# Kernel optimization log

Hardware: AMD Instinct MI355X
Metric: run time of the kernel (lower is better)

Reference implementation:

```python
import jax, jax.numpy as jnp
import numpy as np

HIDDEN, NOISE, MLPW, NCOND, DATA, INIT_NOISE = 64, 16, 128, 4, 8, 16
T, B = 128, 8192
TSCALE = 1.0


def _lipswish(x):
    return 0.909 * x * jax.nn.sigmoid(x)


def _mlp(x, Ws, bs):
    for W, b in zip(Ws[:-1], bs[:-1]):
        x = _lipswish(x @ W + b)
    return TSCALE * jnp.tanh(x @ Ws[-1] + bs[-1])  # tanh regularization, tscale=1.0


def setup_inputs():
    key = jax.random.key(0)
    ks = jax.random.split(key, 12)

    def lin(k, fi, fo):
        k1, k2 = jax.random.split(k)
        lim = 1.0 / float(np.sqrt(fi))
        W = jax.random.uniform(k1, (fi, fo), minval=-lim, maxval=lim, dtype=jnp.float32)
        b = jax.random.uniform(k2, (fo,), minval=-lim, maxval=lim, dtype=jnp.float32)
        return W, b

    ind = 1 + HIDDEN + NCOND  # cat([t, x, c0])
    dr_W0, dr_b0 = lin(ks[0], ind, MLPW)
    dr_W1, dr_b1 = lin(ks[1], MLPW, MLPW)
    dr_W2, dr_b2 = lin(ks[2], MLPW, HIDDEN)
    di_W0, di_b0 = lin(ks[3], ind, MLPW)
    di_W1, di_b1 = lin(ks[4], MLPW, MLPW)
    di_W2, di_b2 = lin(ks[5], MLPW, HIDDEN * NOISE)
    init_W, init_b = lin(ks[6], INIT_NOISE + NCOND, HIDDEN)
    ro_W, ro_b = lin(ks[7], HIDDEN + NCOND, DATA)

    ts = jnp.linspace(0.0, 1.0, T, dtype=jnp.float32)
    dt = 1.0 / (T - 1)
    dW = jax.random.normal(ks[8], (T - 1, B, NOISE), dtype=jnp.float32) * float(np.sqrt(dt))
    conditions = jax.random.normal(ks[9], (NCOND,), dtype=jnp.float32)
    return dict(ts=ts, conditions=conditions, dW=dW,
                dr_W0=dr_W0, dr_b0=dr_b0, dr_W1=dr_W1, dr_b1=dr_b1, dr_W2=dr_W2, dr_b2=dr_b2,
                di_W0=di_W0, di_b0=di_b0, di_W1=di_W1, di_b1=di_b1, di_W2=di_W2, di_b2=di_b2,
                init_W=init_W, init_b=init_b, ro_W=ro_W, ro_b=ro_b, batch_size=B)


def reference(ts, conditions, dW, dr_W0, dr_b0, dr_W1, dr_b1, dr_W2, dr_b2,
              di_W0, di_b0, di_W1, di_b1, di_W2, di_b2, init_W, init_b, ro_W, ro_b,
              batch_size):
    drWs, drbs = (dr_W0, dr_W1, dr_W2), (dr_b0, dr_b1, dr_b2)
    diWs, dibs = (di_W0, di_W1, di_W2), (di_b0, di_b1, di_b2)

    h0 = jnp.ones((batch_size, INIT_NOISE), jnp.float32)  # fixed=True initial point
    c0 = jnp.broadcast_to(conditions[None, :], (batch_size, NCOND))
    x0 = jnp.concatenate([h0, c0], 1) @ init_W + init_b  # (B, H)

    def fg(t, x):
        tcol = jnp.full((x.shape[0], 1), t, x.dtype)
        tx = jnp.concatenate([tcol, x, c0], 1)
        f = _mlp(tx, drWs, drbs)  # (B, H)
        g = _mlp(tx, diWs, dibs).reshape(x.shape[0], HIDDEN, NOISE)  # (B, H, M)
        return f, g

    f0, g0 = fg(ts[0], x0)
    dts = jnp.diff(ts)

    def step(carry, inp):
        y, z, fz, gz = carry
        t1, dt, dw = inp
        # reversible Heun (Stratonovich): auxiliary state z, re-used (f,g) at (t_n, z_n)
        z1 = 2.0 * y - z + fz * dt + jnp.einsum('bhm,bm->bh', gz, dw)
        f1, g1 = fg(t1, z1)
        y1 = y + 0.5 * dt * (fz + f1) + 0.5 * jnp.einsum('bhm,bm->bh', gz + g1, dw)
        return (y1, z1, f1, g1), y1

    _, ys = jax.lax.scan(step, (x0, x0, f0, g0), (ts[1:], dts, dW))
    xs = jnp.concatenate([x0[None], ys], 0).transpose(1, 0, 2)  # (B, T, H)
    nT = xs.shape[1]
    cs = jnp.broadcast_to(c0[:, None, :], (batch_size, nT, NCOND))
    out = jnp.concatenate([xs, cs], -1) @ ro_W + ro_b  # (B, T, data)
    ts_e = jnp.broadcast_to(ts[None, :, None], (batch_size, nT, 1))
    # linear_interpolation_coeffs with no NaNs is the identity on the values
    return jnp.concatenate([ts_e, out], -1)  # (B, T, 1 + data)
```

## Files before the change

kernel.cpp:

```cpp
#include <hip/hip_runtime.h>
#include <hip/hip_bf16.h>
#include <cstdint>
#include <cstddef>

#define B_TOT   8192
#define T_TOT   128
#define ROWS    32
#define THREADS 1024
#define DT      (1.0f/127.0f)

typedef __bf16 bf16x8 __attribute__((ext_vector_type(8)));
typedef float  f32x4  __attribute__((ext_vector_type(4)));

#define WSF_X0    0
#define WSF_BCD   64
#define WSF_BCG   192
#define WSF_ROB   320
#define WSB_SMALL 1536
#define WSB_WD2   (WSB_SMALL + 49152*2)
#define WSB_WG2   (WSB_WD2 + 8192*2)
#define WSB_ROWP  (WSB_WG2 + 131072*2)
#define WSB_TOTAL (WSB_ROWP + 1024*2)

__device__ __forceinline__ unsigned short f2bf(float v){
  union { float f; unsigned u; } x; x.f = v;
  unsigned r = (x.u + 0x7FFFu + ((x.u >> 16) & 1u)) >> 16;
  return (unsigned short)r;
}
__device__ __forceinline__ unsigned cvtpk(float lo, float hi){
  unsigned r;
  asm("v_cvt_pk_bf16_f32 %0, %1, %2" : "=v"(r) : "v"(lo), "v"(hi));
  return r;
}
__device__ __forceinline__ float fexp2(float x){ return __builtin_amdgcn_exp2f(x); }
__device__ __forceinline__ float frcp (float x){ return __builtin_amdgcn_rcpf(x); }
__device__ __forceinline__ float swishf(float x){
  float e = fexp2(-1.44269504088896340f * x);
  return x * frcp(1.0f + e);
}
__device__ __forceinline__ float tanhfast(float x){
  float e = fexp2(2.88539008177792681f * x);
  return 1.0f - 2.0f * frcp(e + 1.0f);
}
__device__ __forceinline__ f32x4 mfma16(bf16x8 a, bf16x8 b, f32x4 c){
  return __builtin_amdgcn_mfma_f32_16x16x32_bf16(a, b, c, 0, 0, 0);
}

__global__ void prep_kernel(const float* __restrict__ cond,
    const float* __restrict__ drW0, const float* __restrict__ drb0,
    const float* __restrict__ drW1, const float* __restrict__ drW2,
    const float* __restrict__ diW0, const float* __restrict__ dib0,
    const float* __restrict__ diW1, const float* __restrict__ diW2,
    const float* __restrict__ initW, const float* __restrict__ initb,
    const float* __restrict__ roW,  const float* __restrict__ rob,
    char* __restrict__ ws)
{
  float* wsf = (float*)ws;
  unsigned short* wsm = (unsigned short*)(ws + WSB_SMALL);
  unsigned short* wd2 = (unsigned short*)(ws + WSB_WD2);
  unsigned short* wg2 = (unsigned short*)(ws + WSB_WG2);
  unsigned short* rwp = (unsigned short*)(ws + WSB_ROWP);
  int tid = blockIdx.x * blockDim.x + threadIdx.x;
  int nth = gridDim.x * blockDim.x;

  for (int h = tid; h < 64; h += nth){
    float s = initb[h];
    #pragma unroll
    for (int i = 0; i < 16; i++) s += initW[i*64 + h];
    #pragma unroll
    for (int c = 0; c < 4; c++) s += cond[c] * initW[(16+c)*64 + h];
    wsf[WSF_X0 + h] = s;
  }
  for (int j = tid; j < 128; j += nth){
    float sd = drb0[j], sg = dib0[j];
    #pragma unroll
    for (int c = 0; c < 4; c++){
      sd += cond[c] * drW0[(65+c)*128 + j];
      sg += cond[c] * diW0[(65+c)*128 + j];
    }
    wsf[WSF_BCD + j] = sd; wsf[WSF_BCG + j] = sg;
  }
  for (int d = tid; d < 8; d += nth){
    float s = rob[d];
    #pragma unroll
    for (int c = 0; c < 4; c++) s += cond[c] * roW[(64+c)*8 + d];
    wsf[WSF_ROB + d] = s;
  }
  for (int u = tid; u < 49152; u += nth){
    int j = u & 7, lane = (u >> 3) & 63, frag = u >> 9;
    int k8 = ((lane >> 4) << 3) + j, o16 = lane & 15;
    float v;
    if (frag < 16)      { int kc = frag & 1,      ot = frag >> 1;      v = drW0[(1 + kc*32 + k8)*128 + ot*16 + o16]; }
    else if (frag < 48) { int f = frag - 16; int kc = f & 3, ot = f >> 2; v = 0.909f * drW1[(kc*32 + k8)*128 + ot*16 + o16]; }
    else if (frag < 64) { int f = frag - 48; int kc = f & 1, ot = f >> 1; v = diW0[(1 + kc*32 + k8)*128 + ot*16 + o16]; }
    else                { int f = frag - 64; int kc = f & 3, ot = f >> 2; v = 0.909f * diW1[(kc*32 + k8)*128 + ot*16 + o16]; }
    wsm[u] = f2bf(v);
  }
  for (int u = tid; u < 8192; u += nth){
    int j = u & 7, lane = (u >> 3) & 63, frag = u >> 9, kc = frag & 3, ot = frag >> 2;
    wd2[u] = f2bf(0.909f * drW2[(kc*32 + ((lane>>4)<<3) + j)*64 + ot*16 + (lane & 15)]);
  }
  for (int u = tid; u < 131072; u += nth){
    int j = u & 7, lane = (u >> 3) & 63, frag = u >> 9, kc = frag & 3, ot = frag >> 2;
    wg2[u] = f2bf(0.909f * diW2[(kc*32 + ((lane>>4)<<3) + j)*1024 + ot*16 + (lane & 15)]);
  }
  for (int u = tid; u < 1024; u += nth){
    int j = u & 7, lane = (u >> 3) & 63, kc = u >> 9;
    int k = kc*32 + ((lane>>4)<<3) + j, o = lane & 15;
    rwp[u] = (o < 8) ? f2bf(roW[k*8 + o]) : (unsigned short)0;
  }
}

__global__ __launch_bounds__(THREADS) void sde_kernel(
    const float* __restrict__ dW,  const float* __restrict__ tsg,
    const float* __restrict__ drW0, const float* __restrict__ diW0,
    const float* __restrict__ bd1, const float* __restrict__ bg1,
    const float* __restrict__ bd2, const float* __restrict__ bg2,
    const char* __restrict__ ws, float* __restrict__ out)
{
  __shared__ unsigned short smallW[49152];
  __shared__ unsigned short z1buf[2048];
  __shared__ unsigned short ybuf[2][2048];
  __shared__ unsigned short h1d[4096];
  __shared__ unsigned short h1g[4096];
  __shared__ unsigned short h2d[4096];
  __shared__ unsigned short h2g[4096];
  __shared__ float tsbuf[128];
  __shared__ float bcdS[128], bcgS[128];
  __shared__ float wtdS[128], wtgS[128];
  __shared__ float bd1S[128], bg1S[128];
  __shared__ float bd2S[64];
  __shared__ float bg2S[1024];
  __shared__ float dwS[2][640];
  __shared__ float robiasS[8];

  const float* wsf = (const float*)ws;
  const unsigned short* wsSmall = (const unsigned short*)(ws + WSB_SMALL);
  const unsigned short* wsWd2   = (const unsigned short*)(ws + WSB_WD2);
  const unsigned short* wsWg2   = (const unsigned short*)(ws + WSB_WG2);
  const unsigned short* wsRoWp  = (const unsigned short*)(ws + WSB_ROWP);

  const int tid = threadIdx.x;
  const int w  = tid >> 6;
  const int l  = tid & 63;
  const int lg = l >> 4;
  const int li = l & 15;
  const int p  = w >> 3;
  const int ot = w & 7;
  const int B0 = blockIdx.x * ROWS;

  const int aEven = lg*512 + ((li ^ lg) << 4);
  const int aOdd  = aEven ^ 64;
  const int gW    = (ot*2 + (lg>>1)) & 7;
  const int wOff  = (ot*2 + (lg>>1))*512 + ((li ^ gW) << 4) + ((lg & 1) << 3);
  const int sOff1 = (p ? 49152 : 0)     + ot*2048 + l*16;
  const int sOff2 = (p ? 65536 : 16384) + ot*4096 + l*16;

  const int bmU  = w & 1;
  const int hb   = (w >> 1) * 8;
  const int otD  = w >> 2;
  const int rowU = bmU*16 + li;
  const int srcLane = ((((w>>1)&1)*2) + (lg>>1))*16 + li;
  const bool lgOdd  = (lg & 1) != 0;
  const int dOffU = rowU*80 + lg*16;
  const int zOff  = (w>>1)*512 + ((rowU ^ ((w>>1)&7)) << 4) + lg*4;

  {
    const uint4* src = (const uint4*)wsSmall;
    uint4* dst = (uint4*)smallW;
    for (int i = tid; i < 6144; i += THREADS) dst[i] = src[i];
    for (int i = tid; i < 128; i += THREADS){
      tsbuf[i] = tsg[i];
      bcdS[i] = wsf[WSF_BCD + i]; bcgS[i] = wsf[WSF_BCG + i];
      wtdS[i] = drW0[i];          wtgS[i] = diW0[i];
      bd1S[i] = bd1[i];           bg1S[i] = bg1[i];
    }
    for (int i = tid; i < 1024; i += THREADS) bg2S[i] = bg2[i];
    if (tid < 64) bd2S[tid] = bd2[tid];
    if (tid < 8) robiasS[tid] = wsf[WSF_ROB + tid];
    if (tid < 128){
      const float* s0 = dW + (size_t)B0*16;
      *(f32x4*)(dwS[0] + (tid>>2)*20 + (tid&3)*4) = *(const f32x4*)(s0 + tid*4);
    }
  }

  float y[2], z[2], fz[2], az[2];
  #pragma unroll
  for (int e = 0; e < 2; e++){ float v = wsf[WSF_X0 + hb + lg*2 + e]; y[e] = v; z[e] = v; }

  auto writeZ = [&](){ *(unsigned*)((char*)z1buf + zOff) = cvtpk(z[0], z[1]); };
  writeZ();
  { *(unsigned*)((char*)ybuf[0] + zOff) = cvtpk(y[0], y[1]); }
  __syncthreads();

  auto rdfrag = [&](const unsigned short* buf, int kc, int bm) -> bf16x8 {
    int off = ((kc & 1) ? aOdd : aEven) + kc*2048 + bm*256;
    return *(const bf16x8*)((const char*)buf + off);
  };

  auto OUTPROJ = [&](int tcur){
    const unsigned short* Yb = ybuf[tcur & 1];
    f32x4 acc = {0.f,0.f,0.f,0.f};
    #pragma unroll
    for (int kc = 0; kc < 2; kc++){
      bf16x8 rw = *(const bf16x8*)((const char*)wsRoWp + kc*1024 + l*16);
      acc = mfma16(rw, rdfrag(Yb, kc, w), acc);
    }
    const int brow = w*16 + li;
    float* orow = out + (size_t)(B0 + brow)*1152 + (size_t)tcur*9;
    if (lg < 2){
      #pragma unroll
      for (int r = 0; r < 4; r++) orow[1 + lg*4 + r] = acc[r] + robiasS[lg*4 + r];
    } else if (lg == 2){
      orow[0] = tsbuf[tcur];
    }
  };

  auto P1 = [&](int s, int kstage, int par){
    if (kstage >= 0 && tid < 128){
      const float* src = dW + (size_t)kstage*131072 + (size_t)B0*16;
      float* dst = dwS[par];
      *(f32x4*)(dst + (tid>>2)*20 + (tid&3)*4) = *(const f32x4*)(src + tid*4);
    }
    float tval = tsbuf[s];
    f32x4 acc0 = {0.f,0.f,0.f,0.f}, acc1 = {0.f,0.f,0.f,0.f};
    #pragma unroll
    for (int kc = 0; kc < 2; kc++){
      bf16x8 af = *(const bf16x8*)((const char*)smallW + sOff1 + kc*1024);
      acc0 = mfma16(af, rdfrag(z1buf, kc, 0), acc0);
      acc1 = mfma16(af, rdfrag(z1buf, kc, 1), acc1);
    }
    f32x4 bcv = *(const f32x4*)((p ? bcgS : bcdS) + ot*16 + lg*4);
    f32x4 wtv = *(const f32x4*)((p ? wtgS : wtdS) + ot*16 + lg*4);
    unsigned short* hout = p ? h1g : h1d;
    #pragma unroll
    for (int bm = 0; bm < 2; bm++){
      const f32x4& acc = bm ? acc1 : acc0;
      float xx[4];
      #pragma unroll
      for (int r = 0; r < 4; r++) xx[r] = swishf(acc[r] + bcv[r] + tval*wtv[r]);
      uint2 v; v.x = cvtpk(xx[0], xx[1]); v.y = cvtpk(xx[2], xx[3]);
      *(uint2*)((char*)hout + wOff + bm*256) = v;
    }
  };

  auto P2 = [&](){
    const unsigned short* hin  = p ? h1g : h1d;
    unsigned short*       hout = p ? h2g : h2d;
    f32x4 acc0 = {0.f,0.f,0.f,0.f}, acc1 = {0.f,0.f,0.f,0.f};
    #pragma unroll
    for (int kc = 0; kc < 4; kc++){
      bf16x8 af = *(const bf16x8*)((const char*)smallW + sOff2 + kc*1024);
      acc0 = mfma16(af, rdfrag(hin, kc, 0), acc0);
      acc1 = mfma16(af, rdfrag(hin, kc, 1), acc1);
    }
    f32x4 b1v = *(const f32x4*)((p ? bg1S : bd1S) + ot*16 + lg*4);
    #pragma unroll
    for (int bm = 0; bm < 2; bm++){
      const f32x4& acc = bm ? acc1 : acc0;
      float xx[4];
      #pragma unroll
      for (int r = 0; r < 4; r++) xx[r] = swishf(acc[r] + b1v[r]);
      uint2 v; v.x = cvtpk(xx[0], xx[1]); v.y = cvtpk(xx[2], xx[3]);
      *(uint2*)((char*)hout + wOff + bm*256) = v;
    }
  };

  auto P3U = [&](const float* DWC, const float* DWN, int k, bool prol){
    if (!prol && w < 2) OUTPROJ(k);
    bf16x8 gf[4];
    #pragma unroll
    for (int kc = 0; kc < 4; kc++) gf[kc] = rdfrag(h2g, kc, bmU);
    const f32x4 dwcv = *(const f32x4*)((const char*)DWC + dOffU);
    const f32x4 dwnv = *(const f32x4*)((const char*)DWN + dOffU);
    float bK0 = 0.f, bK1 = 0.f, aK0 = 0.f, aK1 = 0.f;
    const char* wgbase = (const char*)wsWg2 + (size_t)hb*4096 + l*16;
    #pragma unroll 1
    for (int o = 0; o < 8; o++){
      const char* wb = wgbase + o*4096;
      f32x4 acc = {0.f,0.f,0.f,0.f};
      acc = mfma16(*(const bf16x8*)(wb       ), gf[0], acc);
      acc = mfma16(*(const bf16x8*)(wb + 1024), gf[1], acc);
      acc = mfma16(*(const bf16x8*)(wb + 2048), gf[2], acc);
      acc = mfma16(*(const bf16x8*)(wb + 3072), gf[3], acc);
      f32x4 bgv = *(const f32x4*)(bg2S + (hb + o)*16 + lg*4);
      float bs = 0.f, as_ = 0.f;
      #pragma unroll
      for (int r = 0; r < 4; r++){
        float g = tanhfast(acc[r] + bgv[r]);
        bs  += g * dwcv[r];
        as_ += g * dwnv[r];
      }
      bs  += __shfl_xor(bs, 16);  bs  += __shfl_xor(bs, 32);
      as_ += __shfl_xor(as_, 16); as_ += __shfl_xor(as_, 32);
      if (lg == (o >> 1)){
        if (o & 1){ bK1 = bs; aK1 = as_; }
        else      { bK0 = bs; aK0 = as_; }
      }
    }
    f32x4 accD = {0.f,0.f,0.f,0.f};
    #pragma unroll
    for (int kc = 0; kc < 4; kc++){
      bf16x8 wf = *(const bf16x8*)((const char*)wsWd2 + otD*4096 + kc*1024 + l*16);
      accD = mfma16(wf, rdfrag(h2d, kc, bmU), accD);
    }
    float X[4];
    {
      f32x4 bdv = *(const f32x4*)(bd2S + otD*16 + lg*4);
      #pragma unroll
      for (int r = 0; r < 4; r++) X[r] = accD[r] + bdv[r];
    }
    float f1v[2];
    #pragma unroll
    for (int e = 0; e < 2; e++){
      float t0 = __shfl(X[e],     srcLane, 64);
      float t1 = __shfl(X[e + 2], srcLane, 64);
      f1v[e] = tanhfast(lgOdd ? t1 : t0);
    }
    float bK[2] = {bK0, bK1}, aK[2] = {aK0, aK1};
    if (prol){
      #pragma unroll
      for (int e = 0; e < 2; e++){
        fz[e] = f1v[e]; az[e] = aK[e];
        z[e] = 2.f*y[e] - z[e] + fz[e]*DT + az[e];
      }
      writeZ();
    } else {
      #pragma unroll
      for (int e = 0; e < 2; e++){
        y[e] += 0.5f*DT*(fz[e] + f1v[e]) + 0.5f*(az[e] + bK[e]);
        fz[e] = f1v[e]; az[e] = aK[e];
      }
      *(unsigned*)((char*)ybuf[(k+1)&1] + zOff) = cvtpk(y[0], y[1]);
      if (k < 126){
        #pragma unroll
        for (int e = 0; e < 2; e++) z[e] = 2.f*y[e] - z[e] + fz[e]*DT + az[e];
        writeZ();
      }
    }
  };

  P1(0, -1, 0);
  __syncthreads();
  P2();
  __syncthreads();
  P3U(dwS[0], dwS[0], -1, true);
  __syncthreads();

  for (int k = 0; k < 127; k++){
    P1(k + 1, (k + 1 < 127) ? (k + 1) : 126, (k + 1) & 1);
    __syncthreads();
    P2();
    __syncthreads();
    P3U(dwS[k & 1], dwS[(k + 1) & 1], k, false);
    __syncthreads();
  }

  if (w < 2) OUTPROJ(127);
}

extern "C" void kernel_launch(void* const* d_in, const int* in_sizes, int n_in,
                              void* d_out, int out_size, void* d_ws, size_t ws_size,
                              hipStream_t stream)
{
  const float* ts   = (const float*)d_in[0];
  const float* cond = (const float*)d_in[1];
  const float* dW   = (const float*)d_in[2];
  const float* drW0 = (const float*)d_in[3];
  const float* drb0 = (const float*)d_in[4];
  const float* drW1 = (const float*)d_in[5];
  const float* drb1 = (const float*)d_in[6];
  const float* drW2 = (const float*)d_in[7];
  const float* drb2 = (const float*)d_in[8];
  const float* diW0 = (const float*)d_in[9];
  const float* dib0 = (const float*)d_in[10];
  const float* diW1 = (const float*)d_in[11];
  const float* dib1 = (const float*)d_in[12];
  const float* diW2 = (const float*)d_in[13];
  const float* dib2 = (const float*)d_in[14];
  const float* initW= (const float*)d_in[15];
  const float* initb= (const float*)d_in[16];
  const float* roW  = (const float*)d_in[17];
  const float* rob  = (const float*)d_in[18];
  char* ws = (char*)d_ws;
  if (ws_size < (size_t)WSB_TOTAL) return;

  prep_kernel<<<dim3(256), dim3(256), 0, stream>>>(
      cond, drW0, drb0, drW1, drW2, diW0, dib0, diW1, diW2,
      initW, initb, roW, rob, ws);
  sde_kernel<<<dim3(256), dim3(THREADS), 0, stream>>>(
      dW, ts, drW0, diW0, drb1, dib1, drb2, dib2, ws, (float*)d_out);
}
```

Baseline: 891.7 us.

## Fold tanh exp2 scale into weights/biases and prefetch diffusion weight fragments

The 2/ln2 factor used by the exp2-based tanh is folded into the last-layer drift and diffusion weights and biases during prep, which removes one multiply per tanh evaluation. The diffusion output loop also software-pipelines its weight fragment loads: the first two fragments for the next iteration are loaded early so global-memory latency overlaps with the MFMAs and tanh work. Scaling the weights before bf16 rounding changes rounding slightly, and the prefetch keeps more values live in registers.

New measurement: 847.7 us. 1.05x faster.

```diff
diff --git a/kernel.cpp b/kernel.cpp
--- a/kernel.cpp
+++ b/kernel.cpp
@@ -8,6 +8,7 @@
 #define ROWS    32
 #define THREADS 1024
 #define DT      (1.0f/127.0f)
+#define TSC2    2.88539008177792681f
 
 typedef __bf16 bf16x8 __attribute__((ext_vector_type(8)));
 typedef float  f32x4  __attribute__((ext_vector_type(4)));
@@ -38,8 +39,8 @@
   float e = fexp2(-1.44269504088896340f * x);
   return x * frcp(1.0f + e);
 }
-__device__ __forceinline__ float tanhfast(float x){
-  float e = fexp2(2.88539008177792681f * x);
+__device__ __forceinline__ float tanh_ns(float xs){
+  float e = fexp2(xs);
   return 1.0f - 2.0f * frcp(e + 1.0f);
 }
 __device__ __forceinline__ f32x4 mfma16(bf16x8 a, bf16x8 b, f32x4 c){
@@ -98,11 +99,11 @@
   }
   for (int u = tid; u < 8192; u += nth){
     int j = u & 7, lane = (u >> 3) & 63, frag = u >> 9, kc = frag & 3, ot = frag >> 2;
-    wd2[u] = f2bf(0.909f * drW2[(kc*32 + ((lane>>4)<<3) + j)*64 + ot*16 + (lane & 15)]);
+    wd2[u] = f2bf(0.909f * TSC2 * drW2[(kc*32 + ((lane>>4)<<3) + j)*64 + ot*16 + (lane & 15)]);
   }
   for (int u = tid; u < 131072; u += nth){
     int j = u & 7, lane = (u >> 3) & 63, frag = u >> 9, kc = frag & 3, ot = frag >> 2;
-    wg2[u] = f2bf(0.909f * diW2[(kc*32 + ((lane>>4)<<3) + j)*1024 + ot*16 + (lane & 15)]);
+    wg2[u] = f2bf(0.909f * TSC2 * diW2[(kc*32 + ((lane>>4)<<3) + j)*1024 + ot*16 + (lane & 15)]);
   }
   for (int u = tid; u < 1024; u += nth){
     int j = u & 7, lane = (u >> 3) & 63, kc = u >> 9;
@@ -175,8 +176,8 @@
       wtdS[i] = drW0[i];          wtgS[i] = diW0[i];
       bd1S[i] = bd1[i];           bg1S[i] = bg1[i];
     }
-    for (int i = tid; i < 1024; i += THREADS) bg2S[i] = bg2[i];
-    if (tid < 64) bd2S[tid] = bd2[tid];
+    for (int i = tid; i < 1024; i += THREADS) bg2S[i] = TSC2 * bg2[i];
+    if (tid < 64) bd2S[tid] = TSC2 * bd2[tid];
     if (tid < 8) robiasS[tid] = wsf[WSF_ROB + tid];
     if (tid < 128){
       const float* s0 = dW + (size_t)B0*16;
@@ -275,19 +276,27 @@
     const f32x4 dwnv = *(const f32x4*)((const char*)DWN + dOffU);
     float bK0 = 0.f, bK1 = 0.f, aK0 = 0.f, aK1 = 0.f;
     const char* wgbase = (const char*)wsWg2 + (size_t)hb*4096 + l*16;
+    bf16x8 fk0 = *(const bf16x8*)(wgbase);
+    bf16x8 fk1 = *(const bf16x8*)(wgbase + 1024);
     #pragma unroll 1
     for (int o = 0; o < 8; o++){
       const char* wb = wgbase + o*4096;
+      bf16x8 fk2 = *(const bf16x8*)(wb + 2048);
+      bf16x8 fk3 = *(const bf16x8*)(wb + 3072);
       f32x4 acc = {0.f,0.f,0.f,0.f};
-      acc = mfma16(*(const bf16x8*)(wb       ), gf[0], acc);
-      acc = mfma16(*(const bf16x8*)(wb + 1024), gf[1], acc);
-      acc = mfma16(*(const bf16x8*)(wb + 2048), gf[2], acc);
-      acc = mfma16(*(const bf16x8*)(wb + 3072), gf[3], acc);
+      acc = mfma16(fk0, gf[0], acc);
+      acc = mfma16(fk1, gf[1], acc);
+      acc = mfma16(fk2, gf[2], acc);
+      acc = mfma16(fk3, gf[3], acc);
+      if (o < 7){
+        fk0 = *(const bf16x8*)(wb + 4096);
+        fk1 = *(const bf16x8*)(wb + 4096 + 1024);
+      }
       f32x4 bgv = *(const f32x4*)(bg2S + (hb + o)*16 + lg*4);
       float bs = 0.f, as_ = 0.f;
       #pragma unroll
       for (int r = 0; r < 4; r++){
-        float g = tanhfast(acc[r] + bgv[r]);
+        float g = tanh_ns(acc[r] + bgv[r]);
         bs  += g * dwcv[r];
         as_ += g * dwnv[r];
       }
@@ -315,7 +324,7 @@
     for (int e = 0; e < 2; e++){
       float t0 = __shfl(X[e],     srcLane, 64);
       float t1 = __shfl(X[e + 2], srcLane, 64);
-      f1v[e] = tanhfast(lgOdd ? t1 : t0);
+      f1v[e] = tanh_ns(lgOdd ? t1 : t0);
     }
     float bK[2] = {bK0, bK1}, aK[2] = {aK0, aK1};
     if (prol){
```
